# Kernel tuning notes

Hardware: AMD Instinct MI355X
Metric: run time of the kernel (lower is better)

The kernel has to match this reference:

```python
import jax, jax.numpy as jnp
import numpy as np

L, H, C, D, B, OUT = 3, 4, 128, 128, 64, 128  # layers, heads, out_ch per head, in_dim, graphs, out_dim
NEG_SLOPE = 0.2
EPS = 1e-5


def _layernorm(x, g, b):
    mu = x.mean(-1, keepdims=True)
    var = ((x - mu) ** 2).mean(-1, keepdims=True)
    return (x - mu) * jax.lax.rsqrt(var + EPS) * g + b


def setup_inputs() -> dict:
    key = jax.random.key(0)
    ks = jax.random.split(key, 20)
    N, E = 50000, 400000
    x = jax.random.normal(ks[0], (N, D), jnp.float32)
    edge_index = jax.random.randint(ks[1], (2, E), 0, N, jnp.int64)
    batch = jnp.sort(jax.random.randint(ks[2], (N,), 0, B, jnp.int64))
    s = 1.0 / np.sqrt(D)
    inp = dict(x=x, edge_index=edge_index, batch=batch)
    inp["Wl"] = jax.random.normal(ks[3], (L, H, C, D), jnp.float32) * s
    inp["bl"] = jnp.zeros((L, H, C), jnp.float32)
    inp["Wr"] = jax.random.normal(ks[4], (L, H, C, D), jnp.float32) * s
    inp["br"] = jnp.zeros((L, H, C), jnp.float32)
    inp["att"] = jax.random.normal(ks[5], (L, H, C), jnp.float32) * (1.0 / np.sqrt(C))
    inp["conv_bias"] = jnp.zeros((L, C), jnp.float32)
    inp["ln_gamma"] = jnp.ones((L, C), jnp.float32)
    inp["ln_beta"] = jnp.zeros((L, C), jnp.float32)
    inp["W1"] = jax.random.normal(ks[6], (2 * C, C), jnp.float32) * (1.0 / np.sqrt(C))
    inp["b1"] = jnp.zeros((2 * C,), jnp.float32)
    inp["W2"] = jax.random.normal(ks[7], (OUT, 2 * C), jnp.float32) * (1.0 / np.sqrt(2 * C))
    inp["b2"] = jnp.zeros((OUT,), jnp.float32)
    inp["og"] = jnp.ones((OUT,), jnp.float32)
    inp["ob"] = jnp.zeros((OUT,), jnp.float32)
    return inp


def reference(x, edge_index, batch, Wl, bl, Wr, br, att, conv_bias, ln_gamma, ln_beta, W1, b1, W2, b2, og, ob):
    N = x.shape[0]
    loops = jnp.arange(N, dtype=edge_index.dtype)
    src = jnp.concatenate([edge_index[0], loops])  # [E+N]
    dst = jnp.concatenate([edge_index[1], loops])
    h = x  # input_proj is Identity (node_feat_dim == hidden_dim)
    for l in range(L):
        xl = jnp.einsum('nd,hcd->nhc', h, Wl[l]) + bl[l]  # [N,H,C]
        xr = jnp.einsum('nd,hcd->nhc', h, Wr[l]) + br[l]
        e = jax.nn.leaky_relu(xl[src] + xr[dst], NEG_SLOPE)  # [E+N,H,C]
        logits = jnp.einsum('ehc,hc->eh', e, att[l])  # [E+N,H]
        m = jax.ops.segment_max(logits, dst, num_segments=N)  # [N,H]
        p = jnp.exp(logits - m[dst])
        denom = jax.ops.segment_sum(p, dst, num_segments=N)
        alpha = p / denom[dst]  # segment softmax (self loops guarantee denom>0)
        out = jax.ops.segment_sum(xl[src] * alpha[:, :, None], dst, num_segments=N)  # [N,H,C]
        out = out.mean(axis=1) + conv_bias[l]  # concat=False -> mean over heads
        out = jax.nn.relu(_layernorm(out, ln_gamma[l], ln_beta[l]))
        h = h + out  # residual
    # global mean pool
    sums = jax.ops.segment_sum(h, batch, num_segments=B)
    cnt = jax.ops.segment_sum(jnp.ones((N,), h.dtype), batch, num_segments=B)
    g = sums / jnp.maximum(cnt, 1.0)[:, None]
    # MLP head + out norm
    g = jax.nn.gelu(g @ W1.T + b1, approximate=False) @ W2.T + b2
    return _layernorm(g, og, ob)
```

## Files before the change

kernel.cpp:

```cpp
#include <hip/hip_runtime.h>
#include <hip/hip_bf16.h>

typedef __bf16 bf16x4 __attribute__((ext_vector_type(4)));
typedef __bf16 bf16x8 __attribute__((ext_vector_type(8)));
typedef float f32x4 __attribute__((ext_vector_type(4)));
typedef float f32x2 __attribute__((ext_vector_type(2)));
typedef unsigned char u8;
typedef unsigned long long u64;

#define EPS 1e-5f

static __device__ __forceinline__ int lower_bound_i(const int* __restrict__ arr, int n, int val) {
  int lo = 0, hi = n;
  while (lo < hi) { int mid = (lo + hi) >> 1; if (arr[mid] < val) lo = mid + 1; else hi = mid; }
  return lo;
}

template <int CTRL>
static __device__ __forceinline__ float dpp_add(float x) {
  int s = __builtin_amdgcn_mov_dpp(__float_as_int(x), CTRL, 0xF, 0xF, true);
  return x + __int_as_float(s);
}
static __device__ __forceinline__ float row16_reduce(float t) {
  t = dpp_add<0xB1>(t);
  t = dpp_add<0x4E>(t);
  t = dpp_add<0x141>(t);
  t = dpp_add<0x140>(t);
  return t;
}

static __device__ __forceinline__ u8 f32_to_fp8(float v) {
  int pk = __builtin_amdgcn_cvt_pk_fp8_f32(v, v, 0, false);
  return (u8)(pk & 0xFF);
}
static __device__ __forceinline__ unsigned pack4_fp8(float a, float b, float c, float d) {
  int w = __builtin_amdgcn_cvt_pk_fp8_f32(a, b, 0, false);
  w = __builtin_amdgcn_cvt_pk_fp8_f32(c, d, w, true);
  return (unsigned)w;
}

__global__ void detect_dtypes(const unsigned* __restrict__ xw, const unsigned* __restrict__ eiw,
                              int* __restrict__ flags) {
  __shared__ int s_bf16, s_i64nz;
  int t = threadIdx.x;
  if (t == 0) { s_bf16 = 0; s_i64nz = 0; }
  __syncthreads();
  unsigned w = xw[t * 97];
  unsigned lo = w & 0xFFFFu;
  unsigned e = (lo >> 7) & 0xFF;
  int looks_bf16 = (lo == 0u) || (e >= 0x6A && e <= 0x86);
  atomicAdd(&s_bf16, looks_bf16);
  int k = t * 1031;
  int nz = (eiw[2 * k + 1] != 0u) ? 1 : 0;
  atomicAdd(&s_i64nz, nz);
  __syncthreads();
  if (t == 0) {
    flags[0] = (s_bf16 >= 192) ? 1 : 0;
    flags[1] = (s_i64nz == 0) ? 1 : 0;
  }
}

__global__ void canon_x(const void* __restrict__ src, float* __restrict__ h_f32,
                        u8* __restrict__ h8, int n4, const int* __restrict__ flags) {
  int i = blockIdx.x * blockDim.x + threadIdx.x;
  if (i >= n4) return;
  float v0, v1, v2, v3;
  if (flags[0]) {
    bf16x4 u = ((const bf16x4*)src)[i];
    v0 = (float)u[0]; v1 = (float)u[1]; v2 = (float)u[2]; v3 = (float)u[3];
  } else {
    float4 u = ((const float4*)src)[i];
    v0 = u.x; v1 = u.y; v2 = u.z; v3 = u.w;
  }
  ((float4*)h_f32)[i] = make_float4(v0, v1, v2, v3);
  ((unsigned*)h8)[i] = pack4_fp8(v0, v1, v2, v3);
}

struct ParamDesc { const void* src[12]; int off[13]; };

__global__ void canon_params(ParamDesc pd, float* __restrict__ dst, const int* __restrict__ flags,
                             int total) {
  int i = blockIdx.x * blockDim.x + threadIdx.x;
  if (i >= total) return;
  int s = 0;
#pragma unroll
  for (int k = 1; k < 12; k++) if (i >= pd.off[k]) s = k;
  int j = i - pd.off[s];
  const void* sp = pd.src[s];
  dst[i] = flags[0] ? (float)((const __bf16*)sp)[j] : ((const float*)sp)[j];
}

__global__ void canon_w8(const void* __restrict__ src, u8* __restrict__ dst, int n,
                         const int* __restrict__ flags) {
  int i = blockIdx.x * blockDim.x + threadIdx.x;
  if (i >= n) return;
  float v = flags[0] ? (float)((const __bf16*)src)[i] : ((const float*)src)[i];
  dst[i] = f32_to_fp8(v);
}

__global__ void canon_ints(const void* __restrict__ ei_src, const void* __restrict__ bat_src,
                           int* __restrict__ ei32, int* __restrict__ bat32,
                           int* __restrict__ deg, int E, int N, const int* __restrict__ flags) {
  int i = blockIdx.x * blockDim.x + threadIdx.x;
  int total = 2 * E + N;
  if (i >= total) return;
  int i64 = flags[1];
  if (i < 2 * E) {
    int v = i64 ? (int)((const long long*)ei_src)[i] : ((const int*)ei_src)[i];
    ei32[i] = v;
    if (i >= E) atomicAdd(&deg[v], 1);
  } else {
    int j = i - 2 * E;
    int v = i64 ? (int)((const long long*)bat_src)[j] : ((const int*)bat_src)[j];
    bat32[j] = v;
    atomicAdd(&deg[j], 1);
  }
}

__global__ __launch_bounds__(256) void block_sums(const int* __restrict__ deg,
                                                  int* __restrict__ bsum, int N) {
  __shared__ int sh[256];
  int i = blockIdx.x * 256 + threadIdx.x;
  int t = threadIdx.x;
  sh[t] = (i < N) ? deg[i] : 0;
  __syncthreads();
  for (int off = 128; off > 0; off >>= 1) {
    if (t < off) sh[t] += sh[t + off];
    __syncthreads();
  }
  if (t == 0) bsum[blockIdx.x] = sh[0];
}

__global__ __launch_bounds__(256) void scan_bsums(const int* __restrict__ bsum,
                                                  int* __restrict__ bpref, int nblocks,
                                                  int* __restrict__ offs, int N) {
  __shared__ int sh[256];
  int t = threadIdx.x;
  int carry = 0;
  for (int base = 0; base < nblocks; base += 256) {
    int idx = base + t;
    int v = (idx < nblocks) ? bsum[idx] : 0;
    sh[t] = v;
    __syncthreads();
    for (int off = 1; off < 256; off <<= 1) {
      int u = (t >= off) ? sh[t - off] : 0;
      __syncthreads();
      sh[t] += u;
      __syncthreads();
    }
    if (idx < nblocks) bpref[idx] = carry + sh[t] - v;
    carry += sh[255];
    __syncthreads();
  }
  if (t == 0) offs[N] = carry;
}

__global__ __launch_bounds__(256) void write_offs(const int* __restrict__ deg,
                                                  const int* __restrict__ bpref,
                                                  int* __restrict__ offs,
                                                  int* __restrict__ cursor, int N) {
  __shared__ int sh[256];
  int i = blockIdx.x * 256 + threadIdx.x;
  int t = threadIdx.x;
  int v = (i < N) ? deg[i] : 0;
  sh[t] = v;
  __syncthreads();
  for (int off = 1; off < 256; off <<= 1) {
    int u = (t >= off) ? sh[t - off] : 0;
    __syncthreads();
    sh[t] += u;
    __syncthreads();
  }
  if (i < N) {
    int ex = bpref[blockIdx.x] + sh[t] - v;
    offs[i] = ex;
    cursor[i] = ex;
  }
}

__global__ void fill_csr(const int* __restrict__ ei, int E, int N,
                         int* __restrict__ cursor, int* __restrict__ csr_src) {
  int e = blockIdx.x * blockDim.x + threadIdx.x;
  if (e >= E + N) return;
  int s, d;
  if (e < E) { s = ei[e]; d = ei[E + e]; } else { s = e - E; d = e - E; }
  int pos = atomicAdd(&cursor[d], 1);
  csr_src[pos] = s * 1024;
}

__global__ __launch_bounds__(256) void gemm_xlr(
    const u8* __restrict__ A8, const u8* __restrict__ Wl8,
    const u8* __restrict__ Wr8, const float* __restrict__ bl,
    const float* __restrict__ br, u8* __restrict__ out8, int Nrows) {
  __shared__ u64 As[128][19];
  __shared__ u64 Ws[128][19];
  const int jb = blockIdx.y;
  const u8* Wbase = (jb < 4) ? (Wl8 + (size_t)jb * 16384) : (Wr8 + (size_t)(jb - 4) * 16384);
  const float* biasbase = (jb < 4) ? (bl + jb * 128) : (br + (jb - 4) * 128);
  const int row0 = blockIdx.x * 128;
  const int tid = threadIdx.x;
  const int lane = tid & 63, wave = tid >> 6;
  const int wm = wave >> 1, wn = wave & 1;

#pragma unroll
  for (int p = 0; p < 4; p++) {
    int r = (tid >> 3) + p * 32;
    int qc = (tid & 7) * 2;
    int gr = row0 + r;
    uint4 av = make_uint4(0, 0, 0, 0);
    if (gr < Nrows) av = *(const uint4*)(A8 + (size_t)gr * 128 + qc * 8);
    As[r][qc]     = ((u64)av.y << 32) | av.x;
    As[r][qc + 1] = ((u64)av.w << 32) | av.z;
    uint4 wv = *(const uint4*)(Wbase + (size_t)r * 128 + qc * 8);
    Ws[r][qc]     = ((u64)wv.y << 32) | wv.x;
    Ws[r][qc + 1] = ((u64)wv.w << 32) | wv.z;
  }
  __syncthreads();

  f32x4 acc[4][4];
#pragma unroll
  for (int mi = 0; mi < 4; mi++)
#pragma unroll
    for (int ni = 0; ni < 4; ni++) acc[mi][ni] = f32x4{0.f, 0.f, 0.f, 0.f};

#pragma unroll
  for (int ks = 0; ks < 4; ks++) {
    int qk = ks * 4 + (lane >> 4);
    long af[4], bf[4];
#pragma unroll
    for (int i = 0; i < 4; i++) {
      af[i] = (long)As[wm * 64 + i * 16 + (lane & 15)][qk];
      bf[i] = (long)Ws[wn * 64 + i * 16 + (lane & 15)][qk];
    }
#pragma unroll
    for (int mi = 0; mi < 4; mi++)
#pragma unroll
      for (int ni = 0; ni < 4; ni++)
        acc[mi][ni] = __builtin_amdgcn_mfma_f32_16x16x32_fp8_fp8(af[mi], bf[ni], acc[mi][ni], 0, 0, 0);
  }

#pragma unroll
  for (int mi = 0; mi < 4; mi++) {
#pragma unroll
    for (int ni = 0; ni < 4; ni++) {
      int col_l = wn * 64 + ni * 16 + (lane & 15);
      int gj = jb * 128 + col_l;
      float bias = biasbase[col_l];
#pragma unroll
      for (int r = 0; r < 4; r++) {
        int row_l = wm * 64 + mi * 16 + (lane >> 4) * 4 + r;
        int gr = row0 + row_l;
        if (gr < Nrows) out8[(size_t)gr * 1024 + gj] = f32_to_fp8(acc[mi][ni][r] + bias);
      }
    }
  }
}

__global__ __launch_bounds__(256) void gat_fused(
    const u8* __restrict__ comb8, const float* __restrict__ att,
    const int* __restrict__ offs, const int* __restrict__ csr_src,
    const float* __restrict__ conv_bias, const float* __restrict__ gamma,
    const float* __restrict__ beta, float* __restrict__ h_f32,
    u8* __restrict__ h8, int N, int store_fp8) {
  int wid = blockIdx.x * 4 + (threadIdx.x >> 6);
  int lane = threadIdx.x & 63;
  if (wid >= N) return;
  int n = wid;
  f32x2 xr2[4], at2[4];
  uint2 wr = *(const uint2*)(comb8 + (size_t)n * 1024 + 512 + lane * 8);
  xr2[0] = __builtin_amdgcn_cvt_pk_f32_fp8(wr.x, false);
  xr2[1] = __builtin_amdgcn_cvt_pk_f32_fp8(wr.x, true);
  xr2[2] = __builtin_amdgcn_cvt_pk_f32_fp8(wr.y, false);
  xr2[3] = __builtin_amdgcn_cvt_pk_f32_fp8(wr.y, true);
  float4 a0 = *(const float4*)(att + lane * 8);
  float4 a1 = *(const float4*)(att + lane * 8 + 4);
  at2[0] = f32x2{a0.x, a0.y}; at2[1] = f32x2{a0.z, a0.w};
  at2[2] = f32x2{a1.x, a1.y}; at2[3] = f32x2{a1.z, a1.w};

  int off0 = offs[n], off1 = offs[n + 1];
  float l = 0.f;
  f32x2 acc2[4];
#pragma unroll
  for (int j = 0; j < 4; j++) acc2[j] = f32x2{0.f, 0.f};

  const u8* lane_base = comb8 + lane * 8;

  auto process = [&](uint2 w) {
    f32x2 x2[4];
    x2[0] = __builtin_amdgcn_cvt_pk_f32_fp8(w.x, false);
    x2[1] = __builtin_amdgcn_cvt_pk_f32_fp8(w.x, true);
    x2[2] = __builtin_amdgcn_cvt_pk_f32_fp8(w.y, false);
    x2[3] = __builtin_amdgcn_cvt_pk_f32_fp8(w.y, true);
    f32x2 t2 = f32x2{0.f, 0.f};
#pragma unroll
    for (int j = 0; j < 4; j++) {
      f32x2 z = x2[j] + xr2[j];
      f32x2 lz = __builtin_elementwise_max(z, 0.2f * z);
      t2 = t2 + lz * at2[j];
    }
    float t = t2[0] + t2[1];
    t = row16_reduce(t);
    t = fminf(fmaxf(t, -60.f), 60.f);
    float p = __expf(t);
    l += p;
    f32x2 p2 = f32x2{p, p};
#pragma unroll
    for (int j = 0; j < 4; j++) acc2[j] = acc2[j] + p2 * x2[j];
  };

  int pos = off0;
  for (; pos + 2 <= off1; pos += 2) {
    int b0 = csr_src[pos], b1 = csr_src[pos + 1];
    uint2 wa = *(const uint2*)(lane_base + (size_t)(unsigned)b0);
    uint2 wb = *(const uint2*)(lane_base + (size_t)(unsigned)b1);
    process(wa);
    process(wb);
  }
  if (pos < off1) {
    int b0 = csr_src[pos];
    uint2 wa = *(const uint2*)(lane_base + (size_t)(unsigned)b0);
    process(wa);
  }

  float invl = 1.0f / fmaxf(l, 1e-30f);
  float acc[8];
#pragma unroll
  for (int j = 0; j < 4; j++) {
    acc[2 * j]     = acc2[j][0] * invl;
    acc[2 * j + 1] = acc2[j][1] * invl;
  }
#pragma unroll
  for (int j = 0; j < 8; j++) {
    acc[j] += __shfl_xor(acc[j], 16);
    acc[j] += __shfl_xor(acc[j], 32);
  }
  int c0 = (lane & 15) * 8;
  float v[8];
  float s = 0.f, s2 = 0.f;
#pragma unroll
  for (int j = 0; j < 8; j++) {
    v[j] = acc[j] * 0.25f + conv_bias[c0 + j];
    s += v[j]; s2 += v[j] * v[j];
  }
  s = row16_reduce(s);
  s2 = row16_reduce(s2);
  float mu = s * (1.f / 128.f);
  float var = fmaxf(s2 * (1.f / 128.f) - mu * mu, 0.f);
  float rs = rsqrtf(var + EPS);
  if (lane < 16) {
    float4 o0, o1;
    float hn[8];
#pragma unroll
    for (int j = 0; j < 8; j++) {
      float o = (v[j] - mu) * rs * gamma[c0 + j] + beta[c0 + j];
      o = o > 0.f ? o : 0.f;
      hn[j] = h_f32[(size_t)n * 128 + c0 + j] + o;
    }
    o0.x = hn[0]; o0.y = hn[1]; o0.z = hn[2]; o0.w = hn[3];
    o1.x = hn[4]; o1.y = hn[5]; o1.z = hn[6]; o1.w = hn[7];
    *(float4*)(h_f32 + (size_t)n * 128 + c0) = o0;
    *(float4*)(h_f32 + (size_t)n * 128 + c0 + 4) = o1;
    if (store_fp8) {
      uint2 pk;
      pk.x = pack4_fp8(hn[0], hn[1], hn[2], hn[3]);
      pk.y = pack4_fp8(hn[4], hn[5], hn[6], hn[7]);
      *(uint2*)(h8 + (size_t)n * 128 + c0) = pk;
    }
  }
}

__global__ __launch_bounds__(128) void pool(const float* __restrict__ h_f32,
                                            const int* __restrict__ batch, int N,
                                            float* __restrict__ g_sum) {
  int g = blockIdx.x >> 3, slice = blockIdx.x & 7;
  int c = threadIdx.x;
  int r0 = lower_bound_i(batch, N, g);
  int r1 = lower_bound_i(batch, N, g + 1);
  int len = r1 - r0;
  if (len <= 0) return;
  int per = (len + 7) / 8;
  int s0 = r0 + slice * per;
  int s1 = min(s0 + per, r1);
  if (s0 >= s1) return;
  float acc = 0.f;
  for (int r = s0; r < s1; r++) acc += h_f32[(size_t)r * 128 + c];
  atomicAdd(&g_sum[g * 128 + c], acc);
}

__global__ __launch_bounds__(256) void mlp_head(
    const float* __restrict__ g_sum, const int* __restrict__ batch, int N,
    const float* __restrict__ W1, const float* __restrict__ b1,
    const float* __restrict__ W2, const float* __restrict__ b2,
    const float* __restrict__ og, const float* __restrict__ ob,
    void* __restrict__ outv, const int* __restrict__ flags) {
  __shared__ float gld[128];
  __shared__ float hid[256];
  __shared__ float olds[128];
  __shared__ float red[2];
  int b = blockIdx.x, t = threadIdx.x;
  int r0 = lower_bound_i(batch, N, b);
  int r1 = lower_bound_i(batch, N, b + 1);
  int len = r1 - r0;
  float cntf = (float)(len < 1 ? 1 : len);
  if (t < 128) gld[t] = g_sum[b * 128 + t] / cntf;
  __syncthreads();
  float sacc = b1[t];
  for (int d = 0; d < 128; d++) sacc = fmaf(gld[d], W1[(size_t)t * 128 + d], sacc);
  hid[t] = 0.5f * sacc * (1.f + erff(sacc * 0.70710678118654752f));
  __syncthreads();
  if (t < 128) {
    float o = b2[t];
    for (int k = 0; k < 256; k++) o = fmaf(hid[k], W2[(size_t)t * 256 + k], o);
    olds[t] = o;
  }
  __syncthreads();
  if (t < 64) {
    float a = olds[t], bb = olds[t + 64];
    float s = a + bb, s2 = a * a + bb * bb;
    for (int off = 32; off; off >>= 1) { s += __shfl_down(s, off); s2 += __shfl_down(s2, off); }
    if (t == 0) { red[0] = s * (1.f / 128.f); red[1] = s2 * (1.f / 128.f); }
  }
  __syncthreads();
  if (t < 128) {
    float mu = red[0];
    float var = fmaxf(red[1] - mu * mu, 0.f);
    float rs = rsqrtf(var + EPS);
    float o = (olds[t] - mu) * rs * og[t] + ob[t];
    if (flags[0]) ((__bf16*)outv)[b * 128 + t] = (__bf16)o;
    else          ((float*)outv)[b * 128 + t] = o;
  }
}

extern "C" void kernel_launch(void* const* d_in, const int* in_sizes, int n_in,
                              void* d_out, int out_size, void* d_ws, size_t ws_size,
                              hipStream_t stream) {
  const int D = 128, B = 64;
  const int N = in_sizes[0] / D;
  const int E = in_sizes[1] / 2;
  const int EN = E + N;
  const int nsb = (N + 255) / 256;

  char* p = (char*)d_ws;
  auto alloc = [&](size_t bytes) {
    char* r = p; p += (bytes + 255) & ~(size_t)255; return (void*)r;
  };
  int* flags     = (int*)alloc(256);
  float* h_f32   = (float*)alloc((size_t)N * 128 * 4);
  u8* h8         = (u8*)alloc((size_t)N * 128);
  u8* comb8      = (u8*)alloc((size_t)N * 1024);
  int* deg       = (int*)alloc((size_t)N * 4);
  int* offs      = (int*)alloc((size_t)(N + 1) * 4);
  int* cursor    = (int*)alloc((size_t)N * 4);
  int* csr_src   = (int*)alloc((size_t)EN * 4);
  float* g_sum   = (float*)alloc((size_t)B * 128 * 4);
  int* ei32      = (int*)alloc((size_t)2 * E * 4);
  int* bat32     = (int*)alloc((size_t)N * 4);
  int* bsum      = (int*)alloc((size_t)nsb * 4);
  int* bpref     = (int*)alloc((size_t)nsb * 4);
  u8* w8         = (u8*)alloc((size_t)2 * 196608);
  float* params  = (float*)alloc((size_t)71936 * 4);

  float* bl_c  = params + 0;
  float* br_c  = params + 1536;
  float* att_c = params + 3072;
  float* cb_c  = params + 4608;
  float* g_c   = params + 4992;
  float* b_c   = params + 5376;
  float* W1_c  = params + 5760;
  float* b1_c  = params + 38528;
  float* W2_c  = params + 38784;
  float* b2_c  = params + 71552;
  float* og_c  = params + 71680;
  float* ob_c  = params + 71808;

  detect_dtypes<<<1, 256, 0, stream>>>((const unsigned*)d_in[0], (const unsigned*)d_in[1], flags);

  canon_x<<<(N * 32 + 255) / 256, 256, 0, stream>>>(d_in[0], h_f32, h8, N * 32, flags);

  ParamDesc pd;
  const int srcidx[12] = {4, 6, 7, 8, 9, 10, 11, 12, 13, 14, 15, 16};
  const int sizes12[12] = {1536, 1536, 1536, 384, 384, 384, 32768, 256, 32768, 128, 128, 128};
  int cum = 0;
  for (int k = 0; k < 12; k++) { pd.src[k] = d_in[srcidx[k]]; pd.off[k] = cum; cum += sizes12[k]; }
  pd.off[12] = cum;
  canon_params<<<(cum + 255) / 256, 256, 0, stream>>>(pd, params, flags, cum);

  canon_w8<<<(196608 + 255) / 256, 256, 0, stream>>>(d_in[3], w8, 196608, flags);
  canon_w8<<<(196608 + 255) / 256, 256, 0, stream>>>(d_in[5], w8 + 196608, 196608, flags);

  hipMemsetAsync(deg, 0, (size_t)N * 4, stream);
  hipMemsetAsync(g_sum, 0, (size_t)B * 128 * 4, stream);

  canon_ints<<<(2 * E + N + 255) / 256, 256, 0, stream>>>(d_in[1], d_in[2], ei32, bat32, deg, E, N, flags);
  block_sums<<<nsb, 256, 0, stream>>>(deg, bsum, N);
  scan_bsums<<<1, 256, 0, stream>>>(bsum, bpref, nsb, offs, N);
  write_offs<<<nsb, 256, 0, stream>>>(deg, bpref, offs, cursor, N);
  fill_csr<<<(EN + 255) / 256, 256, 0, stream>>>(ei32, E, N, cursor, csr_src);

  for (int l = 0; l < 3; l++) {
    gemm_xlr<<<dim3((N + 127) / 128, 8), 256, 0, stream>>>(
        h8, w8 + (size_t)l * 65536, w8 + 196608 + (size_t)l * 65536,
        bl_c + l * 512, br_c + l * 512, comb8, N);
    gat_fused<<<(N + 3) / 4, 256, 0, stream>>>(comb8, att_c + l * 512, offs, csr_src,
        cb_c + l * 128, g_c + l * 128, b_c + l * 128, h_f32, h8, N, (l < 2) ? 1 : 0);
  }
  pool<<<B * 8, 128, 0, stream>>>(h_f32, bat32, N, g_sum);
  mlp_head<<<B, 256, 0, stream>>>(g_sum, bat32, N, W1_c, b1_c, W2_c, b2_c, og_c, ob_c, d_out, flags);
}
```

Before: 545.6 us.

## Unroll GAT edge loop by four, vectorize GEMM epilogue stores, merge weight casts

The GAT aggregation loop now handles four edges per iteration and splits scoring from accumulation. This lets four gathers be in flight and four DPP reductions and exps interleave, raising memory-level parallelism. The fp8 GEMM swaps its MFMA operands so each lane holds four consecutive columns, allowing bias to load as a float4 and output to be written as packed 4-byte stores instead of single bytes. The two weight-cast kernel launches are merged into one. The extra registers for four edges in flight may lower occupancy.

```diff
diff --git a/kernel.cpp b/kernel.cpp
--- a/kernel.cpp
+++ b/kernel.cpp
@@ -2,7 +2,6 @@
 #include <hip/hip_bf16.h>
 
 typedef __bf16 bf16x4 __attribute__((ext_vector_type(4)));
-typedef __bf16 bf16x8 __attribute__((ext_vector_type(8)));
 typedef float f32x4 __attribute__((ext_vector_type(4)));
 typedef float f32x2 __attribute__((ext_vector_type(2)));
 typedef unsigned char u8;
@@ -90,11 +89,13 @@
   dst[i] = flags[0] ? (float)((const __bf16*)sp)[j] : ((const float*)sp)[j];
 }
 
-__global__ void canon_w8(const void* __restrict__ src, u8* __restrict__ dst, int n,
-                         const int* __restrict__ flags) {
+__global__ void canon_w8(const void* __restrict__ s1, const void* __restrict__ s2,
+                         u8* __restrict__ dst, int n, const int* __restrict__ flags) {
   int i = blockIdx.x * blockDim.x + threadIdx.x;
-  if (i >= n) return;
-  float v = flags[0] ? (float)((const __bf16*)src)[i] : ((const float*)src)[i];
+  if (i >= 2 * n) return;
+  const void* sp = (i < n) ? s1 : s2;
+  int j = (i < n) ? i : i - n;
+  float v = flags[0] ? (float)((const __bf16*)sp)[j] : ((const float*)sp)[j];
   dst[i] = f32_to_fp8(v);
 }
 
@@ -236,22 +237,20 @@
     for (int mi = 0; mi < 4; mi++)
 #pragma unroll
       for (int ni = 0; ni < 4; ni++)
-        acc[mi][ni] = __builtin_amdgcn_mfma_f32_16x16x32_fp8_fp8(af[mi], bf[ni], acc[mi][ni], 0, 0, 0);
+        acc[mi][ni] = __builtin_amdgcn_mfma_f32_16x16x32_fp8_fp8(bf[ni], af[mi], acc[mi][ni], 0, 0, 0);
   }
 
 #pragma unroll
   for (int mi = 0; mi < 4; mi++) {
+    int gr = row0 + wm * 64 + mi * 16 + (lane & 15);
+    if (gr >= Nrows) continue;
 #pragma unroll
     for (int ni = 0; ni < 4; ni++) {
-      int col_l = wn * 64 + ni * 16 + (lane & 15);
-      int gj = jb * 128 + col_l;
-      float bias = biasbase[col_l];
-#pragma unroll
-      for (int r = 0; r < 4; r++) {
-        int row_l = wm * 64 + mi * 16 + (lane >> 4) * 4 + r;
-        int gr = row0 + row_l;
-        if (gr < Nrows) out8[(size_t)gr * 1024 + gj] = f32_to_fp8(acc[mi][ni][r] + bias);
-      }
+      int col_base = wn * 64 + ni * 16 + (lane >> 4) * 4;
+      float4 b4 = *(const float4*)(biasbase + col_base);
+      unsigned pk = pack4_fp8(acc[mi][ni][0] + b4.x, acc[mi][ni][1] + b4.y,
+                              acc[mi][ni][2] + b4.z, acc[mi][ni][3] + b4.w);
+      *(unsigned*)(out8 + (size_t)gr * 1024 + jb * 128 + col_base) = pk;
     }
   }
 }
@@ -285,7 +284,7 @@
 
   const u8* lane_base = comb8 + lane * 8;
 
-  auto process = [&](uint2 w) {
+  auto edge_dot = [&](uint2 w) -> float {
     f32x2 x2[4];
     x2[0] = __builtin_amdgcn_cvt_pk_f32_fp8(w.x, false);
     x2[1] = __builtin_amdgcn_cvt_pk_f32_fp8(w.x, true);
@@ -298,28 +297,42 @@
       f32x2 lz = __builtin_elementwise_max(z, 0.2f * z);
       t2 = t2 + lz * at2[j];
     }
-    float t = t2[0] + t2[1];
-    t = row16_reduce(t);
-    t = fminf(fmaxf(t, -60.f), 60.f);
-    float p = __expf(t);
-    l += p;
+    return t2[0] + t2[1];
+  };
+  auto accum = [&](uint2 w, float p) {
     f32x2 p2 = f32x2{p, p};
-#pragma unroll
-    for (int j = 0; j < 4; j++) acc2[j] = acc2[j] + p2 * x2[j];
+    f32x2 x;
+    x = __builtin_amdgcn_cvt_pk_f32_fp8(w.x, false); acc2[0] = acc2[0] + p2 * x;
+    x = __builtin_amdgcn_cvt_pk_f32_fp8(w.x, true);  acc2[1] = acc2[1] + p2 * x;
+    x = __builtin_amdgcn_cvt_pk_f32_fp8(w.y, false); acc2[2] = acc2[2] + p2 * x;
+    x = __builtin_amdgcn_cvt_pk_f32_fp8(w.y, true);  acc2[3] = acc2[3] + p2 * x;
   };
 
   int pos = off0;
-  for (; pos + 2 <= off1; pos += 2) {
+  for (; pos + 4 <= off1; pos += 4) {
     int b0 = csr_src[pos], b1 = csr_src[pos + 1];
-    uint2 wa = *(const uint2*)(lane_base + (size_t)(unsigned)b0);
-    uint2 wb = *(const uint2*)(lane_base + (size_t)(unsigned)b1);
-    process(wa);
-    process(wb);
-  }
-  if (pos < off1) {
+    int b2 = csr_src[pos + 2], b3 = csr_src[pos + 3];
+    uint2 w0 = *(const uint2*)(lane_base + (size_t)(unsigned)b0);
+    uint2 w1 = *(const uint2*)(lane_base + (size_t)(unsigned)b1);
+    uint2 w2 = *(const uint2*)(lane_base + (size_t)(unsigned)b2);
+    uint2 w3 = *(const uint2*)(lane_base + (size_t)(unsigned)b3);
+    float t0 = edge_dot(w0), t1 = edge_dot(w1), t2 = edge_dot(w2), t3 = edge_dot(w3);
+    t0 = row16_reduce(t0); t1 = row16_reduce(t1);
+    t2 = row16_reduce(t2); t3 = row16_reduce(t3);
+    t0 = fminf(fmaxf(t0, -60.f), 60.f); t1 = fminf(fmaxf(t1, -60.f), 60.f);
+    t2 = fminf(fmaxf(t2, -60.f), 60.f); t3 = fminf(fmaxf(t3, -60.f), 60.f);
+    float p0 = __expf(t0), p1 = __expf(t1), p2 = __expf(t2), p3 = __expf(t3);
+    l += (p0 + p1) + (p2 + p3);
+    accum(w0, p0); accum(w1, p1); accum(w2, p2); accum(w3, p3);
+  }
+  for (; pos < off1; pos++) {
     int b0 = csr_src[pos];
-    uint2 wa = *(const uint2*)(lane_base + (size_t)(unsigned)b0);
-    process(wa);
+    uint2 w0 = *(const uint2*)(lane_base + (size_t)(unsigned)b0);
+    float t0 = row16_reduce(edge_dot(w0));
+    t0 = fminf(fmaxf(t0, -60.f), 60.f);
+    float p0 = __expf(t0);
+    l += p0;
+    accum(w0, p0);
   }
 
   float invl = 1.0f / fmaxf(l, 1e-30f);
@@ -485,8 +498,7 @@
   pd.off[12] = cum;
   canon_params<<<(cum + 255) / 256, 256, 0, stream>>>(pd, params, flags, cum);
 
-  canon_w8<<<(196608 + 255) / 256, 256, 0, stream>>>(d_in[3], w8, 196608, flags);
-  canon_w8<<<(196608 + 255) / 256, 256, 0, stream>>>(d_in[5], w8 + 196608, 196608, flags);
+  canon_w8<<<(2 * 196608 + 255) / 256, 256, 0, stream>>>(d_in[3], d_in[5], w8, 196608, flags);
 
   hipMemsetAsync(deg, 0, (size_t)N * 4, stream);
   hipMemsetAsync(g_sum, 0, (size_t)B * 128 * 4, stream);
```

New measurement: 565.4 us. 3.6% more time.

## Vectorize GEMM epilogue stores, merge weight casts, fuse pooling into MLP head

Applied to the files above, without the earlier changes.

The FP8 GEMM swaps its MFMA operands so each lane holds four consecutive output columns of one row. The epilogue can then pack them into a single 32-bit store with a vector bias load, replacing four scattered byte stores. The two weight-cast launches are merged into one, and the pooling kernel, its atomics and the g_sum memset are folded into mlp_head, which sums its own graph's rows. The risk is that pooling now runs on only 64 blocks with 2 rows per column step, which could be slower than the 512-block pool.

```diff
diff --git a/kernel.cpp b/kernel.cpp
--- a/kernel.cpp
+++ b/kernel.cpp
@@ -2,7 +2,6 @@
 #include <hip/hip_bf16.h>
 
 typedef __bf16 bf16x4 __attribute__((ext_vector_type(4)));
-typedef __bf16 bf16x8 __attribute__((ext_vector_type(8)));
 typedef float f32x4 __attribute__((ext_vector_type(4)));
 typedef float f32x2 __attribute__((ext_vector_type(2)));
 typedef unsigned char u8;
@@ -90,11 +89,13 @@
   dst[i] = flags[0] ? (float)((const __bf16*)sp)[j] : ((const float*)sp)[j];
 }
 
-__global__ void canon_w8(const void* __restrict__ src, u8* __restrict__ dst, int n,
-                         const int* __restrict__ flags) {
+__global__ void canon_w8(const void* __restrict__ s1, const void* __restrict__ s2,
+                         u8* __restrict__ dst, int n, const int* __restrict__ flags) {
   int i = blockIdx.x * blockDim.x + threadIdx.x;
-  if (i >= n) return;
-  float v = flags[0] ? (float)((const __bf16*)src)[i] : ((const float*)src)[i];
+  if (i >= 2 * n) return;
+  const void* sp = (i < n) ? s1 : s2;
+  int j = (i < n) ? i : i - n;
+  float v = flags[0] ? (float)((const __bf16*)sp)[j] : ((const float*)sp)[j];
   dst[i] = f32_to_fp8(v);
 }
 
@@ -236,22 +237,20 @@
     for (int mi = 0; mi < 4; mi++)
 #pragma unroll
       for (int ni = 0; ni < 4; ni++)
-        acc[mi][ni] = __builtin_amdgcn_mfma_f32_16x16x32_fp8_fp8(af[mi], bf[ni], acc[mi][ni], 0, 0, 0);
+        acc[mi][ni] = __builtin_amdgcn_mfma_f32_16x16x32_fp8_fp8(bf[ni], af[mi], acc[mi][ni], 0, 0, 0);
   }
 
 #pragma unroll
   for (int mi = 0; mi < 4; mi++) {
+    int gr = row0 + wm * 64 + mi * 16 + (lane & 15);
+    if (gr >= Nrows) continue;
 #pragma unroll
     for (int ni = 0; ni < 4; ni++) {
-      int col_l = wn * 64 + ni * 16 + (lane & 15);
-      int gj = jb * 128 + col_l;
-      float bias = biasbase[col_l];
-#pragma unroll
-      for (int r = 0; r < 4; r++) {
-        int row_l = wm * 64 + mi * 16 + (lane >> 4) * 4 + r;
-        int gr = row0 + row_l;
-        if (gr < Nrows) out8[(size_t)gr * 1024 + gj] = f32_to_fp8(acc[mi][ni][r] + bias);
-      }
+      int col_base = wn * 64 + ni * 16 + (lane >> 4) * 4;
+      float4 b4 = *(const float4*)(biasbase + col_base);
+      unsigned pk = pack4_fp8(acc[mi][ni][0] + b4.x, acc[mi][ni][1] + b4.y,
+                              acc[mi][ni][2] + b4.z, acc[mi][ni][3] + b4.w);
+      *(unsigned*)(out8 + (size_t)gr * 1024 + jb * 128 + col_base) = pk;
     }
   }
 }
@@ -369,30 +368,13 @@
   }
 }
 
-__global__ __launch_bounds__(128) void pool(const float* __restrict__ h_f32,
-                                            const int* __restrict__ batch, int N,
-                                            float* __restrict__ g_sum) {
-  int g = blockIdx.x >> 3, slice = blockIdx.x & 7;
-  int c = threadIdx.x;
-  int r0 = lower_bound_i(batch, N, g);
-  int r1 = lower_bound_i(batch, N, g + 1);
-  int len = r1 - r0;
-  if (len <= 0) return;
-  int per = (len + 7) / 8;
-  int s0 = r0 + slice * per;
-  int s1 = min(s0 + per, r1);
-  if (s0 >= s1) return;
-  float acc = 0.f;
-  for (int r = s0; r < s1; r++) acc += h_f32[(size_t)r * 128 + c];
-  atomicAdd(&g_sum[g * 128 + c], acc);
-}
-
 __global__ __launch_bounds__(256) void mlp_head(
-    const float* __restrict__ g_sum, const int* __restrict__ batch, int N,
+    const float* __restrict__ h_f32, const int* __restrict__ batch, int N,
     const float* __restrict__ W1, const float* __restrict__ b1,
     const float* __restrict__ W2, const float* __restrict__ b2,
     const float* __restrict__ og, const float* __restrict__ ob,
     void* __restrict__ outv, const int* __restrict__ flags) {
+  __shared__ float gacc[256];
   __shared__ float gld[128];
   __shared__ float hid[256];
   __shared__ float olds[128];
@@ -402,7 +384,14 @@
   int r1 = lower_bound_i(batch, N, b + 1);
   int len = r1 - r0;
   float cntf = (float)(len < 1 ? 1 : len);
-  if (t < 128) gld[t] = g_sum[b * 128 + t] / cntf;
+  {
+    int c = t & 127, half = t >> 7;
+    float a = 0.f;
+    for (int r = r0 + half; r < r1; r += 2) a += h_f32[(size_t)r * 128 + c];
+    gacc[t] = a;
+  }
+  __syncthreads();
+  if (t < 128) gld[t] = (gacc[t] + gacc[t + 128]) / cntf;
   __syncthreads();
   float sacc = b1[t];
   for (int d = 0; d < 128; d++) sacc = fmaf(gld[d], W1[(size_t)t * 128 + d], sacc);
@@ -452,7 +441,6 @@
   int* offs      = (int*)alloc((size_t)(N + 1) * 4);
   int* cursor    = (int*)alloc((size_t)N * 4);
   int* csr_src   = (int*)alloc((size_t)EN * 4);
-  float* g_sum   = (float*)alloc((size_t)B * 128 * 4);
   int* ei32      = (int*)alloc((size_t)2 * E * 4);
   int* bat32     = (int*)alloc((size_t)N * 4);
   int* bsum      = (int*)alloc((size_t)nsb * 4);
@@ -485,11 +473,9 @@
   pd.off[12] = cum;
   canon_params<<<(cum + 255) / 256, 256, 0, stream>>>(pd, params, flags, cum);
 
-  canon_w8<<<(196608 + 255) / 256, 256, 0, stream>>>(d_in[3], w8, 196608, flags);
-  canon_w8<<<(196608 + 255) / 256, 256, 0, stream>>>(d_in[5], w8 + 196608, 196608, flags);
+  canon_w8<<<(2 * 196608 + 255) / 256, 256, 0, stream>>>(d_in[3], d_in[5], w8, 196608, flags);
 
   hipMemsetAsync(deg, 0, (size_t)N * 4, stream);
-  hipMemsetAsync(g_sum, 0, (size_t)B * 128 * 4, stream);
 
   canon_ints<<<(2 * E + N + 255) / 256, 256, 0, stream>>>(d_in[1], d_in[2], ei32, bat32, deg, E, N, flags);
   block_sums<<<nsb, 256, 0, stream>>>(deg, bsum, N);
@@ -504,6 +490,5 @@
     gat_fused<<<(N + 3) / 4, 256, 0, stream>>>(comb8, att_c + l * 512, offs, csr_src,
         cb_c + l * 128, g_c + l * 128, b_c + l * 128, h_f32, h8, N, (l < 2) ? 1 : 0);
   }
-  pool<<<B * 8, 128, 0, stream>>>(h_f32, bat32, N, g_sum);
-  mlp_head<<<B, 256, 0, stream>>>(g_sum, bat32, N, W1_c, b1_c, W2_c, b2_c, og_c, ob_c, d_out, flags);
-}
+  mlp_head<<<B, 256, 0, stream>>>(h_f32, bat32, N, W1_c, b1_c, W2_c, b2_c, og_c, ob_c, d_out, flags);
+}
```

Result: slower. 600.5 us (+10.1%).
